# Kernel optimization log

Hardware: AMD Instinct MI355X
Metric: run time of the kernel (lower is better)

Reference implementation:

```python
import jax, jax.numpy as jnp
import numpy as np

T, B, D, H = 512, 64, 1024, 1024  # seq_len, batch, input_dim, hidden_dim (must be equal per module)


def setup_inputs() -> dict:
    key = jax.random.key(0)
    ks = jax.random.split(key, 5)
    scale = 1.0 / np.sqrt(D)
    return {
        "x": jax.random.normal(ks[0], (T, B, D), jnp.float32),
        "Wx": jax.random.normal(ks[1], (4, H, D), jnp.float32) * scale,
        "bx": jax.random.normal(ks[2], (4, H), jnp.float32) * scale,
        "Wh": jax.random.normal(ks[3], (4, H, D), jnp.float32) * scale,
        "bh": jax.random.normal(ks[4], (4, H), jnp.float32) * scale,
    }


def reference(x, Wx, bx, Wh, bh):
    # x: [T, B, D]; Wx/Wh: [4, H, D] stacked gates in order (i, f, o, c~); bx/bh: [4, H]
    Tn, Bn, _ = x.shape
    Hn = Wx.shape[1]
    # Precompute all input projections for all 4 gates at once: [T, 4, B, H]
    xproj = jnp.einsum('tbd,ghd->tgbh', x, Wx) + bx[:, None, :]

    def step(carry, xp_t):
        h, c = carry
        g = xp_t + jnp.einsum('bd,ghd->gbh', h, Wh) + bh[:, None, :]  # [4, B, H]
        i = jax.nn.sigmoid(g[0])
        f = jax.nn.sigmoid(g[1])
        o = jax.nn.sigmoid(g[2])
        c_tilde = jnp.tanh(g[3])
        c_new = jax.nn.sigmoid(f * c + i * c_tilde)  # nonstandard sigmoid, faithful to source
        h_new = jnp.tanh(c_new) * o
        return (h_new, c_new), None

    h0 = jnp.zeros((Bn, Hn), x.dtype)
    c0 = jnp.zeros((Bn, Hn), x.dtype)
    (hT, cT), _ = jax.lax.scan(step, (h0, c0), xproj)
    return hT
```

## Files before the change

kernel.cpp:

```cpp
#include <hip/hip_runtime.h>

typedef unsigned short u16;
typedef unsigned int u32;
typedef __attribute__((ext_vector_type(8))) short bf16x8;
typedef __attribute__((ext_vector_type(4))) float f32x4;
typedef const __attribute__((address_space(1))) void* gas1_t;
typedef __attribute__((address_space(3))) void* las3_t;

#define T_LEN 512
#define B_SZ  64
#define D_SZ  1024
#define H_SZ  1024

#define OFF_WX    0UL
#define OFF_WH    8388608UL
#define OFF_BIAS  16777216UL
#define OFF_FLAGS 16793600UL
#define OFF_HROLL 16794624UL
#define OFF_XBF   83903488UL
#define OFF_XPROJ 151012352UL

__device__ __forceinline__ u16 f2bf(float f) {
  u32 u = __builtin_bit_cast(u32, f);
  u += 0x7FFFu + ((u >> 16) & 1u);
  return (u16)(u >> 16);
}
__device__ __forceinline__ float bf2f(u16 h) {
  u32 u = ((u32)h) << 16;
  return __builtin_bit_cast(float, u);
}

__global__ __launch_bounds__(256) void cvt_f32_bf16(const float* __restrict__ in,
                                                    u16* __restrict__ out, int n) {
  int i = (blockIdx.x * 256 + threadIdx.x) * 4;
  if (i >= n) return;
  float4 v = *(const float4*)(in + i);
  ushort4 o;
  o.x = f2bf(v.x); o.y = f2bf(v.y); o.z = f2bf(v.z); o.w = f2bf(v.w);
  *(ushort4*)(out + i) = o;
}

__global__ __launch_bounds__(256) void bias_add(const float* __restrict__ a,
                                                const float* __restrict__ b,
                                                float* __restrict__ o) {
  int i = blockIdx.x * 256 + threadIdx.x;
  o[i] = a[i] + b[i];
}

__global__ __launch_bounds__(256) void gemm_xproj(const u16* __restrict__ A,
                                                  const u16* __restrict__ Bw,
                                                  u16* __restrict__ C) {
  __shared__ __align__(16) u16 As[128 * 64];
  __shared__ __align__(16) u16 Bs[128 * 64];
  int wg = blockIdx.x;
  int swz = (wg & 7) * 1024 + (wg >> 3);
  int mb = swz >> 5;
  int nb = swz & 31;
  int tid = threadIdx.x;
  int lane = tid & 63;
  int w = tid >> 6;
  int wm = w >> 1, wn = w & 1;

  int srow = lane >> 3;
  int scol = (lane & 7) * 8;
  const u16* Abase = A + (size_t)(mb * 128) * 1024;
  const u16* Bbase = Bw + (size_t)(nb * 128) * 1024;

  f32x4 acc[4][4];
#pragma unroll
  for (int i = 0; i < 4; ++i)
#pragma unroll
    for (int j = 0; j < 4; ++j) acc[i][j] = f32x4{0.f, 0.f, 0.f, 0.f};

  for (int k0 = 0; k0 < 1024; k0 += 64) {
#pragma unroll
    for (int r = 0; r < 4; ++r) {
      int chunk = w * 4 + r;
      int row = chunk * 8 + srow;
      __builtin_amdgcn_global_load_lds((gas1_t)(const void*)(Abase + (size_t)row * 1024 + k0 + scol),
                                       (las3_t)(void*)(&As[chunk * 512]), 16, 0, 0);
      __builtin_amdgcn_global_load_lds((gas1_t)(const void*)(Bbase + (size_t)row * 1024 + k0 + scol),
                                       (las3_t)(void*)(&Bs[chunk * 512]), 16, 0, 0);
    }
    __syncthreads();
#pragma unroll
    for (int kk = 0; kk < 64; kk += 32) {
      bf16x8 af[4], bfr[4];
#pragma unroll
      for (int mt = 0; mt < 4; ++mt)
        af[mt] = *(const bf16x8*)&As[(wm * 64 + mt * 16 + (lane & 15)) * 64 + kk + ((lane >> 4) << 3)];
#pragma unroll
      for (int nt = 0; nt < 4; ++nt)
        bfr[nt] = *(const bf16x8*)&Bs[(wn * 64 + nt * 16 + (lane & 15)) * 64 + kk + ((lane >> 4) << 3)];
#pragma unroll
      for (int mt = 0; mt < 4; ++mt)
#pragma unroll
        for (int nt = 0; nt < 4; ++nt)
          acc[mt][nt] = __builtin_amdgcn_mfma_f32_16x16x32_bf16(af[mt], bfr[nt], acc[mt][nt], 0, 0, 0);
    }
    __syncthreads();
  }
  int crowbase = mb * 128 + wm * 64;
  int ccolbase = nb * 128 + wn * 64;
#pragma unroll
  for (int mt = 0; mt < 4; ++mt)
#pragma unroll
    for (int nt = 0; nt < 4; ++nt) {
      int col = ccolbase + nt * 16 + (lane & 15);
      int gate = col >> 10;
      int hc = col & 1023;
      size_t cb = (size_t)gate * 65536 + (size_t)(hc >> 3) * 512 + (hc & 7);
#pragma unroll
      for (int r = 0; r < 4; ++r) {
        int row = crowbase + mt * 16 + ((lane >> 4) << 2) + r;
        C[(size_t)(row >> 6) * 262144 + cb + (size_t)(row & 63) * 8] = f2bf(acc[mt][nt][r]);
      }
    }
}

__global__ __launch_bounds__(512, 2) void lstm_seq(const u16* __restrict__ xprojP,
                                                   const u16* __restrict__ Whb,
                                                   const float* __restrict__ bias,
                                                   u16* __restrict__ hroll,
                                                   u32* __restrict__ flags,
                                                   float* __restrict__ out) {
  __shared__ float pacc[64 * 272];
#define PIDX(frag, row, col) (((frag) * 272) + (row) * 17 + (col))
  int wg = blockIdx.x;
  int bh = wg >> 6;
  int hw = wg & 63;
  int tid = threadIdx.x;
  int lane = tid & 63;
  int kq = tid >> 6;
  int kw = kq << 7;
  int hi8 = (lane >> 4) << 3;

  bf16x8 wf[4][4];
#pragma unroll
  for (int f = 0; f < 4; ++f) {
    int wrow = (f << 10) + (hw << 4) + (lane & 15);
#pragma unroll
    for (int ks = 0; ks < 4; ++ks)
      wf[f][ks] = *(const bf16x8*)&Whb[(size_t)wrow * 1024 + kw + ks * 32 + hi8];
  }

  int b = tid >> 4;
  int jj = tid & 15;
  int hrow = (bh << 5) + b;
  int hcol = (hw << 4) + jj;
  float bs0 = bias[hcol], bs1 = bias[1024 + hcol], bs2 = bias[2048 + hcol], bs3 = bias[3072 + hcol];
  float c_state = 0.f;
  int am_row0 = (bh << 5) + (lane & 15);
  int am_row1 = am_row0 + 16;
  int mI = b >> 4, r16 = b & 15;
  u32* cnt = flags + (bh << 6);

  const u16* xpt = xprojP + (size_t)(hcol >> 3) * 512 + (size_t)hrow * 8 + (hcol & 7);
  u32 px0 = xpt[0], px1 = xpt[65536], px2 = xpt[131072], px3 = xpt[196608];

  for (int t = 0; t < T_LEN; ++t) {
    const u16* hcur = hroll + (size_t)t * 65536;
    const u16* p0 = hcur + (size_t)am_row0 * 1024 + kw + hi8;
    const u16* p1 = hcur + (size_t)am_row1 * 1024 + kw + hi8;
    bf16x8 a0[4], a1[4];
#pragma unroll
    for (int ks = 0; ks < 4; ++ks) {
      a0[ks] = *(const bf16x8*)(p0 + ks * 32);
      a1[ks] = *(const bf16x8*)(p1 + ks * 32);
    }

    f32x4 acc00 = f32x4{0.f, 0.f, 0.f, 0.f}, acc01 = acc00, acc02 = acc00, acc03 = acc00;
    f32x4 acc10 = acc00, acc11 = acc00, acc12 = acc00, acc13 = acc00;
#pragma unroll
    for (int ks = 0; ks < 4; ++ks) {
      acc00 = __builtin_amdgcn_mfma_f32_16x16x32_bf16(a0[ks], wf[0][ks], acc00, 0, 0, 0);
      acc01 = __builtin_amdgcn_mfma_f32_16x16x32_bf16(a0[ks], wf[1][ks], acc01, 0, 0, 0);
      acc02 = __builtin_amdgcn_mfma_f32_16x16x32_bf16(a0[ks], wf[2][ks], acc02, 0, 0, 0);
      acc03 = __builtin_amdgcn_mfma_f32_16x16x32_bf16(a0[ks], wf[3][ks], acc03, 0, 0, 0);
      acc10 = __builtin_amdgcn_mfma_f32_16x16x32_bf16(a1[ks], wf[0][ks], acc10, 0, 0, 0);
      acc11 = __builtin_amdgcn_mfma_f32_16x16x32_bf16(a1[ks], wf[1][ks], acc11, 0, 0, 0);
      acc12 = __builtin_amdgcn_mfma_f32_16x16x32_bf16(a1[ks], wf[2][ks], acc12, 0, 0, 0);
      acc13 = __builtin_amdgcn_mfma_f32_16x16x32_bf16(a1[ks], wf[3][ks], acc13, 0, 0, 0);
    }
    {
      int rbase = (lane >> 4) << 2;
      int cidx = lane & 15;
      int f0i = kq << 3;
#pragma unroll
      for (int r = 0; r < 4; ++r) {
        pacc[PIDX(f0i + 0, rbase + r, cidx)] = acc00[r];
        pacc[PIDX(f0i + 1, rbase + r, cidx)] = acc01[r];
        pacc[PIDX(f0i + 2, rbase + r, cidx)] = acc02[r];
        pacc[PIDX(f0i + 3, rbase + r, cidx)] = acc03[r];
        pacc[PIDX(f0i + 4, rbase + r, cidx)] = acc10[r];
        pacc[PIDX(f0i + 5, rbase + r, cidx)] = acc11[r];
        pacc[PIDX(f0i + 6, rbase + r, cidx)] = acc12[r];
        pacc[PIDX(f0i + 7, rbase + r, cidx)] = acc13[r];
      }
    }
    __syncthreads();
    float g[4];
#pragma unroll
    for (int f = 0; f < 4; ++f) {
      float s = 0.f;
#pragma unroll
      for (int k2 = 0; k2 < 8; ++k2)
        s += pacc[PIDX((k2 << 3) + (mI << 2) + f, r16, jj)];
      g[f] = s;
    }
    asm volatile("s_waitcnt vmcnt(0)" : "+v"(px0), "+v"(px1), "+v"(px2), "+v"(px3));
    float gi = g[0] + bf2f((u16)px0) + bs0;
    float gf = g[1] + bf2f((u16)px1) + bs1;
    float go = g[2] + bf2f((u16)px2) + bs2;
    float gc = g[3] + bf2f((u16)px3) + bs3;
    float iv = 1.f / (1.f + __expf(-gi));
    float fv = 1.f / (1.f + __expf(-gf));
    float ov = 1.f / (1.f + __expf(-go));
    float cv = tanhf(gc);
    c_state = 1.f / (1.f + __expf(-(fv * c_state + iv * cv)));
    float hn = tanhf(c_state) * ov;

    if (t == T_LEN - 1) {
      out[(size_t)hrow * 1024 + hcol] = hn;
    } else {
      u16* hdst = hroll + (size_t)(t + 1) * 65536 + (size_t)hrow * 1024 + hcol;
      const u16* xn0 = xpt + (size_t)(t + 1) * 262144;
      const u16* xn1 = xn0 + 65536;
      const u16* xn2 = xn0 + 131072;
      const u16* xn3 = xn0 + 196608;
      u32 hb = (u32)f2bf(hn);
      asm volatile(
          "global_store_short %4, %9, off sc0 sc1\n\t"
          "global_load_ushort %0, %5, off\n\t"
          "global_load_ushort %1, %6, off\n\t"
          "global_load_ushort %2, %7, off\n\t"
          "global_load_ushort %3, %8, off\n\t"
          "s_waitcnt vmcnt(4)"
          : "=&v"(px0), "=&v"(px1), "=&v"(px2), "=&v"(px3)
          : "v"(hdst), "v"(xn0), "v"(xn1), "v"(xn2), "v"(xn3), "v"(hb)
          : "memory");
      __syncthreads();
      if (tid == 0) {
        u32 one = 1u;
        asm volatile("global_atomic_add %0, %1, off" :: "v"(cnt), "v"(one) : "memory");
        u32 tgt = (u32)((t + 1) << 6);
        u32 f;
        for (;;) {
          asm volatile("global_load_dword %0, %1, off sc0 sc1\n\ts_waitcnt vmcnt(0)"
                       : "=&v"(f) : "v"(cnt) : "memory");
          if (f >= tgt) break;
        }
      }
      __syncthreads();
    }
  }
}

extern "C" void kernel_launch(void* const* d_in, const int* in_sizes, int n_in,
                              void* d_out, int out_size, void* d_ws, size_t ws_size,
                              hipStream_t stream) {
  const float* x  = (const float*)d_in[0];
  const float* Wx = (const float*)d_in[1];
  const float* bx = (const float*)d_in[2];
  const float* Wh = (const float*)d_in[3];
  const float* bh = (const float*)d_in[4];
  float* out = (float*)d_out;
  char* ws = (char*)d_ws;

  u16* wx_bf  = (u16*)(ws + OFF_WX);
  u16* wh_bf  = (u16*)(ws + OFF_WH);
  float* bias = (float*)(ws + OFF_BIAS);
  u32* flags  = (u32*)(ws + OFF_FLAGS);
  u16* hroll  = (u16*)(ws + OFF_HROLL);
  u16* x_bf   = (u16*)(ws + OFF_XBF);
  u16* xproj  = (u16*)(ws + OFF_XPROJ);

  hipMemsetAsync(ws + OFF_FLAGS, 0, 1024 + 131072, stream);

  cvt_f32_bf16<<<4096, 256, 0, stream>>>(Wx, wx_bf, 4194304);
  cvt_f32_bf16<<<4096, 256, 0, stream>>>(Wh, wh_bf, 4194304);
  bias_add<<<16, 256, 0, stream>>>(bx, bh, bias);
  cvt_f32_bf16<<<32768, 256, 0, stream>>>(x, x_bf, 33554432);
  gemm_xproj<<<8192, 256, 0, stream>>>(x_bf, wx_bf, xproj);
  lstm_seq<<<128, 512, 0, stream>>>(xproj, wh_bf, bias, hroll, flags, out);
}
```

Before: 3.291 ms.

## Fuse input-projection GEMM into recurrent kernel with producer/consumer flag sync

Merges the x-projection GEMM and the sequential LSTM recurrence into one persistent launch. 128 extra workgroups compute xproj tiles in time order and bump per-timestep-pair counters, while the 128 recurrence workgroups poll those counters before reading xproj. The aim is to hide the large upfront GEMM behind the latency-bound recurrence. The cost is extra polling, smaller GEMM tiles with one loop per tile, and reliance on all 256 workgroups being resident at once to avoid deadlock.

```diff
diff --git a/kernel.cpp b/kernel.cpp
--- a/kernel.cpp
+++ b/kernel.cpp
@@ -4,6 +4,7 @@
 typedef unsigned int u32;
 typedef __attribute__((ext_vector_type(8))) short bf16x8;
 typedef __attribute__((ext_vector_type(4))) float f32x4;
+typedef __attribute__((ext_vector_type(4))) u32 u32x4;
 typedef const __attribute__((address_space(1))) void* gas1_t;
 typedef __attribute__((address_space(3))) void* las3_t;
 
@@ -16,9 +17,9 @@
 #define OFF_WH    8388608UL
 #define OFF_BIAS  16777216UL
 #define OFF_FLAGS 16793600UL
-#define OFF_HROLL 16794624UL
-#define OFF_XBF   83903488UL
-#define OFF_XPROJ 151012352UL
+#define OFF_HROLL 16795648UL
+#define OFF_XBF   83904512UL
+#define OFF_XPROJ 151013376UL
 
 __device__ __forceinline__ u16 f2bf(float f) {
   u32 u = __builtin_bit_cast(u32, f);
@@ -47,93 +48,103 @@
   o[i] = a[i] + b[i];
 }
 
-__global__ __launch_bounds__(256) void gemm_xproj(const u16* __restrict__ A,
-                                                  const u16* __restrict__ Bw,
-                                                  u16* __restrict__ C) {
-  __shared__ __align__(16) u16 As[128 * 64];
-  __shared__ __align__(16) u16 Bs[128 * 64];
+__global__ __launch_bounds__(512, 2) void lstm_fused(const u16* __restrict__ A,
+                                                     const u16* __restrict__ Bw,
+                                                     u16* __restrict__ xprojP,
+                                                     const u16* __restrict__ Whb,
+                                                     const float* __restrict__ bias,
+                                                     u16* __restrict__ hroll,
+                                                     u32* __restrict__ flags,
+                                                     float* __restrict__ out) {
+  __shared__ __align__(16) char smem[69632];
   int wg = blockIdx.x;
-  int swz = (wg & 7) * 1024 + (wg >> 3);
-  int mb = swz >> 5;
-  int nb = swz & 31;
   int tid = threadIdx.x;
   int lane = tid & 63;
   int w = tid >> 6;
-  int wm = w >> 1, wn = w & 1;
-
-  int srow = lane >> 3;
-  int scol = (lane & 7) * 8;
-  const u16* Abase = A + (size_t)(mb * 128) * 1024;
-  const u16* Bbase = Bw + (size_t)(nb * 128) * 1024;
-
-  f32x4 acc[4][4];
-#pragma unroll
-  for (int i = 0; i < 4; ++i)
-#pragma unroll
-    for (int j = 0; j < 4; ++j) acc[i][j] = f32x4{0.f, 0.f, 0.f, 0.f};
-
-  for (int k0 = 0; k0 < 1024; k0 += 64) {
-#pragma unroll
-    for (int r = 0; r < 4; ++r) {
-      int chunk = w * 4 + r;
-      int row = chunk * 8 + srow;
-      __builtin_amdgcn_global_load_lds((gas1_t)(const void*)(Abase + (size_t)row * 1024 + k0 + scol),
-                                       (las3_t)(void*)(&As[chunk * 512]), 16, 0, 0);
-      __builtin_amdgcn_global_load_lds((gas1_t)(const void*)(Bbase + (size_t)row * 1024 + k0 + scol),
-                                       (las3_t)(void*)(&Bs[chunk * 512]), 16, 0, 0);
-    }
-    __syncthreads();
-#pragma unroll
-    for (int kk = 0; kk < 64; kk += 32) {
-      bf16x8 af[4], bfr[4];
-#pragma unroll
-      for (int mt = 0; mt < 4; ++mt)
-        af[mt] = *(const bf16x8*)&As[(wm * 64 + mt * 16 + (lane & 15)) * 64 + kk + ((lane >> 4) << 3)];
-#pragma unroll
-      for (int nt = 0; nt < 4; ++nt)
-        bfr[nt] = *(const bf16x8*)&Bs[(wn * 64 + nt * 16 + (lane & 15)) * 64 + kk + ((lane >> 4) << 3)];
-#pragma unroll
-      for (int mt = 0; mt < 4; ++mt)
-#pragma unroll
-        for (int nt = 0; nt < 4; ++nt)
-          acc[mt][nt] = __builtin_amdgcn_mfma_f32_16x16x32_bf16(af[mt], bfr[nt], acc[mt][nt], 0, 0, 0);
-    }
-    __syncthreads();
+  int hi8 = (lane >> 4) << 3;
+  u32* cntx = flags + 256;
+
+  if (wg >= 128) {
+    u16* As = (u16*)smem;
+    u16* Bs = (u16*)(smem + 16384);
+    int g = wg - 128;
+    int wm = w >> 1, wn = w & 1;
+    int col8 = (lane & 7) * 8;
+    int rowL = w * 8 + (lane >> 3);
+
+    for (int idx = g; idx < 8192; idx += 128) {
+      int tp = idx >> 5;
+      int nb = idx & 31;
+      const u16* At = A + (size_t)tp * 131072;
+      const u16* Bt = Bw + (size_t)nb * 131072;
+
+      f32x4 acc[2][4];
+#pragma unroll
+      for (int mt = 0; mt < 2; ++mt)
+#pragma unroll
+        for (int nt = 0; nt < 4; ++nt) acc[mt][nt] = f32x4{0.f, 0.f, 0.f, 0.f};
+
+      for (int k0 = 0; k0 < 1024; k0 += 64) {
+#pragma unroll
+        for (int r = 0; r < 2; ++r) {
+          int row = r * 64 + rowL;
+          int dst = r * 4096 + w * 512;
+          __builtin_amdgcn_global_load_lds((gas1_t)(const void*)(At + (size_t)row * 1024 + k0 + col8),
+                                           (las3_t)(void*)(&As[dst]), 16, 0, 0);
+          __builtin_amdgcn_global_load_lds((gas1_t)(const void*)(Bt + (size_t)row * 1024 + k0 + col8),
+                                           (las3_t)(void*)(&Bs[dst]), 16, 0, 0);
+        }
+        __syncthreads();
+#pragma unroll
+        for (int kk = 0; kk < 64; kk += 32) {
+          bf16x8 af[2], bfr[4];
+#pragma unroll
+          for (int mt = 0; mt < 2; ++mt)
+            af[mt] = *(const bf16x8*)&As[(wm * 32 + mt * 16 + (lane & 15)) * 64 + kk + hi8];
+#pragma unroll
+          for (int nt = 0; nt < 4; ++nt)
+            bfr[nt] = *(const bf16x8*)&Bs[(wn * 64 + nt * 16 + (lane & 15)) * 64 + kk + hi8];
+#pragma unroll
+          for (int mt = 0; mt < 2; ++mt)
+#pragma unroll
+            for (int nt = 0; nt < 4; ++nt)
+              acc[mt][nt] = __builtin_amdgcn_mfma_f32_16x16x32_bf16(af[mt], bfr[nt], acc[mt][nt], 0, 0, 0);
+        }
+        __syncthreads();
+      }
+#pragma unroll
+      for (int mt = 0; mt < 2; ++mt)
+#pragma unroll
+        for (int nt = 0; nt < 4; ++nt) {
+          int col = nb * 128 + wn * 64 + nt * 16 + (lane & 15);
+          int gate = col >> 10;
+          int hc = col & 1023;
+          size_t cb = (size_t)gate * 65536 + (size_t)(hc >> 3) * 512 + (hc & 7);
+#pragma unroll
+          for (int r = 0; r < 4; ++r) {
+            int row = tp * 128 + wm * 32 + mt * 16 + ((lane >> 4) << 2) + r;
+            u16* cp = xprojP + (size_t)(row >> 6) * 262144 + cb + (size_t)(row & 63) * 8;
+            u32 val = (u32)f2bf(acc[mt][nt][r]);
+            asm volatile("global_store_short %0, %1, off sc0 sc1" :: "v"(cp), "v"(val) : "memory");
+          }
+        }
+      asm volatile("s_waitcnt vmcnt(0)" ::: "memory");
+      __syncthreads();
+      if (tid == 0) {
+        u32 one = 1u;
+        u32* cp = cntx + tp;
+        asm volatile("global_atomic_add %0, %1, off" :: "v"(cp), "v"(one) : "memory");
+      }
+    }
+    return;
   }
-  int crowbase = mb * 128 + wm * 64;
-  int ccolbase = nb * 128 + wn * 64;
-#pragma unroll
-  for (int mt = 0; mt < 4; ++mt)
-#pragma unroll
-    for (int nt = 0; nt < 4; ++nt) {
-      int col = ccolbase + nt * 16 + (lane & 15);
-      int gate = col >> 10;
-      int hc = col & 1023;
-      size_t cb = (size_t)gate * 65536 + (size_t)(hc >> 3) * 512 + (hc & 7);
-#pragma unroll
-      for (int r = 0; r < 4; ++r) {
-        int row = crowbase + mt * 16 + ((lane >> 4) << 2) + r;
-        C[(size_t)(row >> 6) * 262144 + cb + (size_t)(row & 63) * 8] = f2bf(acc[mt][nt][r]);
-      }
-    }
-}
-
-__global__ __launch_bounds__(512, 2) void lstm_seq(const u16* __restrict__ xprojP,
-                                                   const u16* __restrict__ Whb,
-                                                   const float* __restrict__ bias,
-                                                   u16* __restrict__ hroll,
-                                                   u32* __restrict__ flags,
-                                                   float* __restrict__ out) {
-  __shared__ float pacc[64 * 272];
+
+  float* pacc = (float*)smem;
 #define PIDX(frag, row, col) (((frag) * 272) + (row) * 17 + (col))
-  int wg = blockIdx.x;
   int bh = wg >> 6;
   int hw = wg & 63;
-  int tid = threadIdx.x;
-  int lane = tid & 63;
-  int kq = tid >> 6;
+  int kq = w;
   int kw = kq << 7;
-  int hi8 = (lane >> 4) << 3;
 
   bf16x8 wf[4][4];
 #pragma unroll
@@ -156,6 +167,23 @@
   u32* cnt = flags + (bh << 6);
 
   const u16* xpt = xprojP + (size_t)(hcol >> 3) * 512 + (size_t)hrow * 8 + (hcol & 7);
+  int ready_tp = 0;
+
+  {
+    const u32* cp = cntx;
+    for (;;) {
+      u32x4 c4;
+      asm volatile("global_load_dwordx4 %0, %1, off sc0 sc1\n\ts_waitcnt vmcnt(0)"
+                   : "=&v"(c4) : "v"(cp) : "memory");
+      if (c4[0] >= 32u) {
+        ready_tp = 1;
+        if (c4[1] >= 32u) { ready_tp = 2;
+          if (c4[2] >= 32u) { ready_tp = 3;
+            if (c4[3] >= 32u) ready_tp = 4; } }
+        break;
+      }
+    }
+  }
   u32 px0 = xpt[0], px1 = xpt[65536], px2 = xpt[131072], px3 = xpt[196608];
 
   for (int t = 0; t < T_LEN; ++t) {
@@ -224,21 +252,41 @@
       out[(size_t)hrow * 1024 + hcol] = hn;
     } else {
       u16* hdst = hroll + (size_t)(t + 1) * 65536 + (size_t)hrow * 1024 + hcol;
+      u32 hb = (u32)f2bf(hn);
+      asm volatile("global_store_short %0, %1, off sc0 sc1" :: "v"(hdst), "v"(hb) : "memory");
+      int tpn = (t + 1) >> 1;
+      if (tpn >= ready_tp) {
+        const u32* cp = cntx + (tpn & ~3);
+        int q = tpn & 3;
+        for (;;) {
+          u32x4 c4;
+          asm volatile("global_load_dwordx4 %0, %1, off sc0 sc1\n\ts_waitcnt vmcnt(0)"
+                       : "=&v"(c4) : "v"(cp) : "memory");
+          u32 v0 = c4[0], v1 = c4[1], v2 = c4[2], v3 = c4[3];
+          bool b0 = v0 >= 32u, b1 = v1 >= 32u, b2 = v2 >= 32u, b3 = v3 >= 32u;
+          bool mine = (q == 0) ? b0 : (q == 1) ? b1 : (q == 2) ? b2 : b3;
+          if (mine) {
+            int ext = (q == 0) ? (b1 ? (b2 ? (b3 ? 4 : 3) : 2) : 1)
+                    : (q == 1) ? (b2 ? (b3 ? 3 : 2) : 1)
+                    : (q == 2) ? (b3 ? 2 : 1) : 1;
+            ready_tp = tpn + ext;
+            break;
+          }
+        }
+      }
       const u16* xn0 = xpt + (size_t)(t + 1) * 262144;
       const u16* xn1 = xn0 + 65536;
       const u16* xn2 = xn0 + 131072;
       const u16* xn3 = xn0 + 196608;
-      u32 hb = (u32)f2bf(hn);
       asm volatile(
-          "global_store_short %4, %9, off sc0 sc1\n\t"
-          "global_load_ushort %0, %5, off\n\t"
-          "global_load_ushort %1, %6, off\n\t"
-          "global_load_ushort %2, %7, off\n\t"
-          "global_load_ushort %3, %8, off\n\t"
-          "s_waitcnt vmcnt(4)"
+          "global_load_ushort %0, %4, off\n\t"
+          "global_load_ushort %1, %5, off\n\t"
+          "global_load_ushort %2, %6, off\n\t"
+          "global_load_ushort %3, %7, off"
           : "=&v"(px0), "=&v"(px1), "=&v"(px2), "=&v"(px3)
-          : "v"(hdst), "v"(xn0), "v"(xn1), "v"(xn2), "v"(xn3), "v"(hb)
+          : "v"(xn0), "v"(xn1), "v"(xn2), "v"(xn3)
           : "memory");
+      asm volatile("s_waitcnt vmcnt(4)" ::: "memory");
       __syncthreads();
       if (tid == 0) {
         u32 one = 1u;
@@ -275,12 +323,11 @@
   u16* x_bf   = (u16*)(ws + OFF_XBF);
   u16* xproj  = (u16*)(ws + OFF_XPROJ);
 
-  hipMemsetAsync(ws + OFF_FLAGS, 0, 1024 + 131072, stream);
+  hipMemsetAsync(ws + OFF_FLAGS, 0, 2048 + 131072, stream);
 
   cvt_f32_bf16<<<4096, 256, 0, stream>>>(Wx, wx_bf, 4194304);
   cvt_f32_bf16<<<4096, 256, 0, stream>>>(Wh, wh_bf, 4194304);
   bias_add<<<16, 256, 0, stream>>>(bx, bh, bias);
   cvt_f32_bf16<<<32768, 256, 0, stream>>>(x, x_bf, 33554432);
-  gemm_xproj<<<8192, 256, 0, stream>>>(x_bf, wx_bf, xproj);
-  lstm_seq<<<128, 512, 0, stream>>>(xproj, wh_bf, bias, hroll, flags, out);
-}
+  lstm_fused<<<256, 512, 0, stream>>>(x_bf, wx_bf, xproj, wh_bf, bias, hroll, flags, out);
+}
```

Result: faster. 2.851 ms (median of 2 runs) (-13.4%).
